# Optimization experiments

Measured on AMD Instinct MI355X. Metric: run time of the kernel, lower is better.

## Reference

```python
import jax, jax.numpy as jnp
import numpy as np

NUM_C = 10000
SEQ_LEN = 1024
EMB = 512
HEADS = 8
NUM_EN = 2
B = 8
HEAD_DIM = EMB // HEADS


def _ln(x, s, b, eps=1e-5):
    m = jnp.mean(x, -1, keepdims=True)
    v = jnp.mean((x - m) ** 2, -1, keepdims=True)
    return (x - m) / jnp.sqrt(v + eps) * s + b


def setup_inputs():
    key = jax.random.key(0)
    k = jax.random.split(key, 16)

    def n(i, shape, scale=0.02):
        return scale * jax.random.normal(k[i], shape, dtype=jnp.float32)

    q = jax.random.randint(k[0], (B, SEQ_LEN), 0, NUM_C)
    r = jax.random.randint(k[1], (B, SEQ_LEN), 0, 2)
    qry = jax.random.randint(k[2], (B, SEQ_LEN), 0, NUM_C)
    alphas = n(3, (SEQ_LEN, 2), 0.001)
    # gumbels = -log(Exp(1) + eps), matching torch's exponential_() sampling
    gumbel = -jnp.log(jax.random.exponential(k[4], (SEQ_LEN, 2), dtype=jnp.float32) + 1e-5)
    # keep offset-0 (the diagonal band) selected so no attention row is fully masked
    gumbel = gumbel.at[0, 0].set(10.0)
    return {
        "q": q, "r": r, "qry": qry,
        "alphas": alphas, "gumbel": gumbel,
        "inter_emb": n(5, (2 * NUM_C, EMB)),
        "ex_emb": n(6, (NUM_C, EMB)),
        "pos_emb": n(7, (SEQ_LEN, EMB)),
        "Wqkv": n(8, (NUM_EN, 3 * EMB, EMB)),
        "bqkv": jnp.zeros((NUM_EN, 3 * EMB), jnp.float32),
        "Wo": n(9, (NUM_EN, EMB, EMB)),
        "bo": jnp.zeros((NUM_EN, EMB), jnp.float32),
        "ln1_s": jnp.ones((NUM_EN, EMB), jnp.float32),
        "ln1_b": jnp.zeros((NUM_EN, EMB), jnp.float32),
        "W1": n(10, (NUM_EN, EMB, EMB)),
        "b1": jnp.zeros((NUM_EN, EMB), jnp.float32),
        "W2": n(11, (NUM_EN, EMB, EMB)),
        "b2": jnp.zeros((NUM_EN, EMB), jnp.float32),
        "ln2_s": jnp.ones((NUM_EN, EMB), jnp.float32),
        "ln2_b": jnp.zeros((NUM_EN, EMB), jnp.float32),
        "pred_w": n(12, (1, EMB)),
        "pred_b": jnp.zeros((1,), jnp.float32),
    }


def reference(q, r, qry, alphas, gumbel, inter_emb, ex_emb, pos_emb, Wqkv, bqkv, Wo, bo,
              ln1_s, ln1_b, W1, b1, W2, b2, ln2_s, ln2_b, pred_w, pred_b):
    L = SEQ_LEN
    x = inter_emb[q + NUM_C * r] + pos_emb[jnp.arange(L)]  # [B,L,E]
    qsh = ex_emb[qry]                                      # [B,L,E]

    # Gumbel-softmax hard top-1 (straight-through); column 0 == "keep" indicator per offset
    y_soft = jax.nn.softmax(alphas + gumbel, axis=-1)      # tau = 1
    y_hard = jax.nn.one_hot(jnp.argmax(y_soft, -1), 2, dtype=y_soft.dtype)
    m = (y_hard - jax.lax.stop_gradient(y_soft) + y_soft)[:, 0]  # [L], 0/1 in fwd

    # The triu/rot90/loop construction collapses to a symmetric Toeplitz: dam[i,j] = m[|i-j|]
    idx = jnp.arange(L)
    dam = m[jnp.abs(idx[:, None] - idx[None, :])]          # [L,L]
    allowed = (idx[None, :] <= idx[:, None]) & (dam != 0)  # causal AND band kept
    bias = jnp.where(allowed, 0.0, -jnp.inf)               # same for all heads

    scale = np.float32(1.0 / np.sqrt(HEAD_DIM))
    for l in range(NUM_EN):
        Wq, Wk, Wv = jnp.split(Wqkv[l], 3, axis=0)
        bq, bk, bv = jnp.split(bqkv[l], 3, axis=0)
        qp = (qsh @ Wq.T + bq).reshape(B, L, HEADS, HEAD_DIM)
        kp = (x @ Wk.T + bk).reshape(B, L, HEADS, HEAD_DIM)
        vp = (x @ Wv.T + bv).reshape(B, L, HEADS, HEAD_DIM)
        scores = jnp.einsum('bihd,bjhd->bhij', qp, kp) * scale + bias
        attn = jax.nn.softmax(scores, axis=-1)
        out = jnp.einsum('bhij,bjhd->bihd', attn, vp).reshape(B, L, EMB)
        out = out @ Wo[l].T + bo[l]
        h = _ln(qsh + out, ln1_s[l], ln1_b[l])             # residual with the query (as in source)
        ff = jax.nn.relu(h @ W1[l].T + b1[l]) @ W2[l].T + b2[l]
        x = _ln(h + ff, ln2_s[l], ln2_b[l])

    p = jax.nn.sigmoid(x @ pred_w.T + pred_b).squeeze(-1)  # [B,L]
    mask_L1 = jnp.sum(jnp.abs(alphas))
    return p, mask_L1
```

## Files before the change

kernel.cpp:

```cpp
#include <hip/hip_runtime.h>
#include <hip/hip_bf16.h>

#define L_SEQ 1024
#define NUMC  10000

typedef __attribute__((ext_vector_type(8))) short bf16x8;
typedef __attribute__((ext_vector_type(4))) float f32x4;

__device__ __forceinline__ unsigned int bf2(float a, float b) {
    unsigned int ua = __float_as_uint(a);
    ua = (ua + 0x7fffu + ((ua >> 16) & 1u)) >> 16;
    unsigned int ub = __float_as_uint(b);
    ub = (ub + 0x7fffu + ((ub >> 16) & 1u)) >> 16;
    return ua | (ub << 16);
}
__device__ __forceinline__ unsigned short bf1(float a) {
    unsigned int ua = __float_as_uint(a);
    return (unsigned short)((ua + 0x7fffu + ((ua >> 16) & 1u)) >> 16);
}

__global__ __launch_bounds__(256) void mask_l1_kernel(
    const float* __restrict__ alphas, const float* __restrict__ gumbel,
    float* __restrict__ msk, float* __restrict__ out)
{
    int tid = threadIdx.x;
    float la = 0.0f;
    #pragma unroll
    for (int rr = 0; rr < 4; ++rr) {
        int i = tid + rr * 256;
        float a0 = alphas[2*i],  a1 = alphas[2*i+1];
        float s0 = a0 + gumbel[2*i], s1 = a1 + gumbel[2*i+1];
        msk[i] = (s0 >= s1) ? 1.0f : 0.0f;
        la += fabsf(a0) + fabsf(a1);
    }
    #pragma unroll
    for (int o = 1; o < 64; o <<= 1) la += __shfl_xor(la, o);
    __shared__ float red[4];
    int lane = tid & 63, wid = tid >> 6;
    if (lane == 0) red[wid] = la;
    __syncthreads();
    if (tid == 0)
        out[8192] = red[0] + red[1] + red[2] + red[3];
}

__global__ __launch_bounds__(128) void embed_x_kernel(
    const int* __restrict__ q, const int* __restrict__ r,
    const float* __restrict__ inter_emb, const float* __restrict__ pos_emb,
    float* __restrict__ x)
{
    int row = blockIdx.x;
    int pos = row & (L_SEQ - 1);
    int t = threadIdx.x;
    int e = q[row] + NUMC * r[row];
    float4 a = ((const float4*)(inter_emb + (size_t)e * 512))[t];
    float4 p = ((const float4*)(pos_emb + (size_t)pos * 512))[t];
    float4 o; o.x=a.x+p.x; o.y=a.y+p.y; o.z=a.z+p.z; o.w=a.w+p.w;
    ((float4*)(x + (size_t)row * 512))[t] = o;
}

__global__ __launch_bounds__(128) void embed_q_kernel(
    const int* __restrict__ qry, const float* __restrict__ ex_emb,
    float* __restrict__ qsh)
{
    int row = blockIdx.x;
    int t = threadIdx.x;
    ((float4*)(qsh + (size_t)row * 512))[t] =
        ((const float4*)(ex_emb + (size_t)qry[row] * 512))[t];
}

__global__ __launch_bounds__(256) void gemm_mfma(
    const float* __restrict__ A, const float* __restrict__ W,
    const float* __restrict__ bias, const float* __restrict__ R,
    void* __restrict__ C_, int c_bf, int ldc, int relu)
{
    __shared__ __align__(16) char lsA[128 * 128];
    __shared__ __align__(16) char lsB[128 * 128];
    int t = threadIdx.x;
    int lane = t & 63, wid = t >> 6;
    int wr = wid >> 1, wc = wid & 1;
    int l15 = lane & 15, l4 = lane >> 4;
    int m0 = blockIdx.y * 128, n0 = blockIdx.x * 128;

    f32x4 zero = {0.f, 0.f, 0.f, 0.f};
    f32x4 acc[4][4];
    #pragma unroll
    for (int i = 0; i < 4; ++i)
        #pragma unroll
        for (int j = 0; j < 4; ++j) acc[i][j] = zero;

    for (int kt = 0; kt < 512; kt += 64) {
        float4 ra[4][2], rb[4][2];
        #pragma unroll
        for (int i = 0; i < 4; ++i) {
            int pp = t + (i << 8);
            int row = pp >> 3, c8 = pp & 7;
            const float* pa = A + (size_t)(m0 + row) * 512 + kt + (c8 << 3);
            ra[i][0] = *(const float4*)pa;
            ra[i][1] = *(const float4*)(pa + 4);
            const float* pb = W + (size_t)(n0 + row) * 512 + kt + (c8 << 3);
            rb[i][0] = *(const float4*)pb;
            rb[i][1] = *(const float4*)(pb + 4);
        }
        __syncthreads();
        #pragma unroll
        for (int i = 0; i < 4; ++i) {
            int pp = t + (i << 8);
            int row = pp >> 3, c8 = pp & 7;
            int byte = ((row << 7) + (c8 << 4)) ^ ((row & 7) << 4);
            uint4 pk;
            pk.x = bf2(ra[i][0].x, ra[i][0].y);
            pk.y = bf2(ra[i][0].z, ra[i][0].w);
            pk.z = bf2(ra[i][1].x, ra[i][1].y);
            pk.w = bf2(ra[i][1].z, ra[i][1].w);
            *(uint4*)(lsA + byte) = pk;
            pk.x = bf2(rb[i][0].x, rb[i][0].y);
            pk.y = bf2(rb[i][0].z, rb[i][0].w);
            pk.z = bf2(rb[i][1].x, rb[i][1].y);
            pk.w = bf2(rb[i][1].z, rb[i][1].w);
            *(uint4*)(lsB + byte) = pk;
        }
        __syncthreads();
        #pragma unroll
        for (int kk = 0; kk < 2; ++kk) {
            bf16x8 af[4], bfv[4];
            #pragma unroll
            for (int i = 0; i < 4; ++i) {
                int rowA = (wr << 6) + (i << 4) + l15;
                int ba = ((rowA << 7) + (kk << 6) + (l4 << 4)) ^ ((rowA & 7) << 4);
                af[i] = *(const bf16x8*)(lsA + ba);
                int rowB = (wc << 6) + (i << 4) + l15;
                int bb = ((rowB << 7) + (kk << 6) + (l4 << 4)) ^ ((rowB & 7) << 4);
                bfv[i] = *(const bf16x8*)(lsB + bb);
            }
            #pragma unroll
            for (int i = 0; i < 4; ++i)
                #pragma unroll
                for (int j = 0; j < 4; ++j)
                    acc[i][j] = __builtin_amdgcn_mfma_f32_16x16x32_bf16(
                        af[i], bfv[j], acc[i][j], 0, 0, 0);
        }
    }
    float bv[4];
    #pragma unroll
    for (int j = 0; j < 4; ++j) bv[j] = bias[n0 + (wc << 6) + (j << 4) + l15];
    #pragma unroll
    for (int i = 0; i < 4; ++i) {
        #pragma unroll
        for (int r = 0; r < 4; ++r) {
            int grow = m0 + (wr << 6) + (i << 4) + (l4 << 2) + r;
            #pragma unroll
            for (int j = 0; j < 4; ++j) {
                int gcol = n0 + (wc << 6) + (j << 4) + l15;
                float o = acc[i][j][r] + bv[j];
                if (R) o += R[(size_t)grow * 512 + gcol];
                if (relu) o = fmaxf(o, 0.0f);
                if (c_bf) ((__hip_bfloat16*)C_)[(size_t)grow * ldc + gcol] = __float2bfloat16(o);
                else      ((float*)C_)[(size_t)grow * ldc + gcol] = o;
            }
        }
    }
}

__global__ __launch_bounds__(256) void attn_mfma(
    const float* __restrict__ qsh, const float* __restrict__ Wq,
    const float* __restrict__ bq, const __hip_bfloat16* __restrict__ KV,
    const float* __restrict__ msk, float* __restrict__ O)
{
    __shared__ __align__(16) char lsK[64 * 128];
    __shared__ __align__(16) char lsV[64 * 128];
    __shared__ __align__(16) char lsQ[64 * 128];
    __shared__ __align__(16) char lsP[64 * 128];
    __shared__ float mskS[L_SEQ];
    int qt = blockIdx.x, h = blockIdx.y, b = blockIdx.z;
    int i0 = qt * 64;
    size_t base = (size_t)b * L_SEQ;
    int t = threadIdx.x;
    int lane = t & 63, w = t >> 6, l15 = lane & 15, l4 = lane >> 4;

    #pragma unroll
    for (int k = 0; k < 4; ++k) mskS[t + k * 256] = msk[t + k * 256];

    f32x4 zero = {0.f, 0.f, 0.f, 0.f};
    f32x4 qa[4];
    #pragma unroll
    for (int j = 0; j < 4; ++j) qa[j] = zero;
    for (int kt = 0; kt < 512; kt += 64) {
        float4 ra[2][2], rb[2][2];
        #pragma unroll
        for (int i = 0; i < 2; ++i) {
            int p = t * 2 + i;
            int row = p >> 3, c8 = p & 7;
            const float* pa = qsh + (base + i0 + row) * 512 + kt + (c8 << 3);
            ra[i][0] = *(const float4*)pa;  ra[i][1] = *(const float4*)(pa + 4);
            const float* pw = Wq + (size_t)(h * 64 + row) * 512 + kt + (c8 << 3);
            rb[i][0] = *(const float4*)pw;  rb[i][1] = *(const float4*)(pw + 4);
        }
        __syncthreads();
        #pragma unroll
        for (int i = 0; i < 2; ++i) {
            int p = t * 2 + i;
            int row = p >> 3, c8 = p & 7;
            int byte = ((row << 7) + (c8 << 4)) ^ ((row & 7) << 4);
            uint4 pk;
            pk.x = bf2(ra[i][0].x, ra[i][0].y); pk.y = bf2(ra[i][0].z, ra[i][0].w);
            pk.z = bf2(ra[i][1].x, ra[i][1].y); pk.w = bf2(ra[i][1].z, ra[i][1].w);
            *(uint4*)(lsK + byte) = pk;
            pk.x = bf2(rb[i][0].x, rb[i][0].y); pk.y = bf2(rb[i][0].z, rb[i][0].w);
            pk.z = bf2(rb[i][1].x, rb[i][1].y); pk.w = bf2(rb[i][1].z, rb[i][1].w);
            *(uint4*)(lsV + byte) = pk;
        }
        __syncthreads();
        #pragma unroll
        for (int kk = 0; kk < 2; ++kk) {
            int ra_ = (w << 4) + l15;
            bf16x8 af = *(const bf16x8*)(lsK + (((ra_ << 7) + (kk << 6) + (l4 << 4)) ^ ((ra_ & 7) << 4)));
            #pragma unroll
            for (int df = 0; df < 4; ++df) {
                int rb_ = (df << 4) + l15;
                bf16x8 bf = *(const bf16x8*)(lsV + (((rb_ << 7) + (kk << 6) + (l4 << 4)) ^ ((rb_ & 7) << 4)));
                qa[df] = __builtin_amdgcn_mfma_f32_16x16x32_bf16(af, bf, qa[df], 0, 0, 0);
            }
        }
    }
    #pragma unroll
    for (int df = 0; df < 4; ++df) {
        float bias = bq[h * 64 + (df << 4) + l15];
        #pragma unroll
        for (int r = 0; r < 4; ++r) {
            int row = (w << 4) + (l4 << 2) + r;
            int byte = ((row << 7) + (((df << 4) + l15) << 1)) ^ ((row & 7) << 4);
            *(unsigned short*)(lsQ + byte) = bf1(qa[df][r] + bias);
        }
    }

    float mcur[4], lcur[4];
    f32x4 oa[4];
    #pragma unroll
    for (int r = 0; r < 4; ++r) { mcur[r] = -INFINITY; lcur[r] = 0.f; }
    #pragma unroll
    for (int df = 0; df < 4; ++df) oa[df] = zero;

    for (int jt = 0; jt <= qt; ++jt) {
        int j0 = jt * 64;
        __syncthreads();
        #pragma unroll
        for (int i = 0; i < 2; ++i) {
            int p = t * 2 + i;
            int row = p >> 3, c8 = p & 7;
            uint4 kv4 = *(const uint4*)(KV + (base + j0 + row) * 1024 + h * 64 + (c8 << 3));
            *(uint4*)(lsK + (((row << 7) + (c8 << 4)) ^ ((row & 7) << 4))) = kv4;
            uint4 vv = *(const uint4*)(KV + (base + j0 + row) * 1024 + 512 + h * 64 + (c8 << 3));
            const unsigned short* vs = (const unsigned short*)&vv;
            #pragma unroll
            for (int e = 0; e < 8; ++e) {
                int d = (c8 << 3) + e;
                *(unsigned short*)(lsV + (((d << 7) + (row << 1)) ^ ((d & 7) << 4))) = vs[e];
            }
        }
        __syncthreads();
        f32x4 s[4];
        #pragma unroll
        for (int jf = 0; jf < 4; ++jf) s[jf] = zero;
        #pragma unroll
        for (int kk = 0; kk < 2; ++kk) {
            int ra_ = (w << 4) + l15;
            bf16x8 af = *(const bf16x8*)(lsQ + (((ra_ << 7) + (kk << 6) + (l4 << 4)) ^ ((ra_ & 7) << 4)));
            #pragma unroll
            for (int jf = 0; jf < 4; ++jf) {
                int rb_ = (jf << 4) + l15;
                bf16x8 bf = *(const bf16x8*)(lsK + (((rb_ << 7) + (kk << 6) + (l4 << 4)) ^ ((rb_ & 7) << 4)));
                s[jf] = __builtin_amdgcn_mfma_f32_16x16x32_bf16(af, bf, s[jf], 0, 0, 0);
            }
        }
        #pragma unroll
        for (int r = 0; r < 4; ++r) {
            int gi = i0 + (w << 4) + (l4 << 2) + r;
            float rm = -INFINITY;
            #pragma unroll
            for (int jf = 0; jf < 4; ++jf) {
                int gj = j0 + (jf << 4) + l15;
                float v = s[jf][r] * 0.125f;
                bool ok = (gj <= gi) && (mskS[gi - gj] != 0.0f);
                v = ok ? v : -INFINITY;
                s[jf][r] = v;
                rm = fmaxf(rm, v);
            }
            #pragma unroll
            for (int o = 1; o < 16; o <<= 1) rm = fmaxf(rm, __shfl_xor(rm, o));
            float mn = fmaxf(mcur[r], rm);
            float c, psum = 0.f;
            if (mn == -INFINITY) {
                c = 1.0f;
                #pragma unroll
                for (int jf = 0; jf < 4; ++jf) s[jf][r] = 0.f;
            } else {
                c = __expf(mcur[r] - mn);
                #pragma unroll
                for (int jf = 0; jf < 4; ++jf) {
                    float e = __expf(s[jf][r] - mn);
                    s[jf][r] = e; psum += e;
                }
            }
            #pragma unroll
            for (int o = 1; o < 16; o <<= 1) psum += __shfl_xor(psum, o);
            mcur[r] = mn;
            lcur[r] = lcur[r] * c + psum;
            #pragma unroll
            for (int df = 0; df < 4; ++df) oa[df][r] *= c;
            int row = (w << 4) + (l4 << 2) + r;
            #pragma unroll
            for (int jf = 0; jf < 4; ++jf) {
                int byte = ((row << 7) + (((jf << 4) + l15) << 1)) ^ ((row & 7) << 4);
                *(unsigned short*)(lsP + byte) = bf1(s[jf][r]);
            }
        }
        __syncthreads();
        #pragma unroll
        for (int kk = 0; kk < 2; ++kk) {
            int ra_ = (w << 4) + l15;
            bf16x8 pf = *(const bf16x8*)(lsP + (((ra_ << 7) + (kk << 6) + (l4 << 4)) ^ ((ra_ & 7) << 4)));
            #pragma unroll
            for (int df = 0; df < 4; ++df) {
                int rb_ = (df << 4) + l15;
                bf16x8 vf = *(const bf16x8*)(lsV + (((rb_ << 7) + (kk << 6) + (l4 << 4)) ^ ((rb_ & 7) << 4)));
                oa[df] = __builtin_amdgcn_mfma_f32_16x16x32_bf16(pf, vf, oa[df], 0, 0, 0);
            }
        }
    }
    #pragma unroll
    for (int r = 0; r < 4; ++r) {
        int gi = i0 + (w << 4) + (l4 << 2) + r;
        float inv = 1.0f / lcur[r];
        #pragma unroll
        for (int df = 0; df < 4; ++df)
            O[(base + gi) * 512 + h * 64 + (df << 4) + l15] = oa[df][r] * inv;
    }
}

__global__ __launch_bounds__(128) void ln_kernel(float* __restrict__ X,
    const float* __restrict__ s, const float* __restrict__ b)
{
    int row = blockIdx.x, t = threadIdx.x;
    float* xp = X + (size_t)row * 512;
    float4 v = *((float4*)xp + t);
    float ps = v.x + v.y + v.z + v.w;
    #pragma unroll
    for (int o = 1; o < 64; o <<= 1) ps += __shfl_xor(ps, o);
    __shared__ float sm[4];
    int lane = t & 63, wid = t >> 6;
    if (lane == 0) sm[wid] = ps;
    __syncthreads();
    float mean = (sm[0] + sm[1]) * (1.0f / 512.0f);
    float4 d; d.x=v.x-mean; d.y=v.y-mean; d.z=v.z-mean; d.w=v.w-mean;
    float sq = d.x*d.x + d.y*d.y + d.z*d.z + d.w*d.w;
    #pragma unroll
    for (int o = 1; o < 64; o <<= 1) sq += __shfl_xor(sq, o);
    if (lane == 0) sm[2 + wid] = sq;
    __syncthreads();
    float inv = rsqrtf((sm[2] + sm[3]) * (1.0f / 512.0f) + 1e-5f);
    float4 sc = *((const float4*)s + t);
    float4 sh = *((const float4*)b + t);
    float4 o;
    o.x = d.x*inv*sc.x + sh.x; o.y = d.y*inv*sc.y + sh.y;
    o.z = d.z*inv*sc.z + sh.z; o.w = d.w*inv*sc.w + sh.w;
    *((float4*)xp + t) = o;
}

__global__ __launch_bounds__(256) void desakt_50629074485961_kernel(
    const float* __restrict__ x, const float* __restrict__ pw,
    const float* __restrict__ pb, float* __restrict__ out)
{
    int row = blockIdx.x * 4 + (threadIdx.x >> 6);
    int lane = threadIdx.x & 63;
    const float4* xr = (const float4*)(x + (size_t)row * 512) + lane * 2;
    const float4* wr = (const float4*)pw + lane * 2;
    float4 a0 = xr[0], a1 = xr[1], w0 = wr[0], w1 = wr[1];
    float s = a0.x*w0.x + a0.y*w0.y + a0.z*w0.z + a0.w*w0.w
            + a1.x*w1.x + a1.y*w1.y + a1.z*w1.z + a1.w*w1.w;
    #pragma unroll
    for (int o = 1; o < 64; o <<= 1) s += __shfl_xor(s, o);
    if (lane == 0) {
        float z = s + pb[0];
        out[row] = 1.0f / (1.0f + __expf(-z));
    }
}

extern "C" __attribute__((visibility("default")))
void kernel_launch(void* const* d_in, const int* in_sizes, int n_in,
                   void* d_out, int out_size, void* d_ws, size_t ws_size,
                   hipStream_t stream) {
    (void)in_sizes; (void)n_in; (void)out_size;
    const int*   q        = (const int*)d_in[0];
    const int*   r        = (const int*)d_in[1];
    const int*   qry      = (const int*)d_in[2];
    const float* alphas   = (const float*)d_in[3];
    const float* gumbel   = (const float*)d_in[4];
    const float* inter_emb= (const float*)d_in[5];
    const float* ex_emb   = (const float*)d_in[6];
    const float* pos_emb  = (const float*)d_in[7];
    const float* Wqkv     = (const float*)d_in[8];
    const float* bqkv     = (const float*)d_in[9];
    const float* Wo       = (const float*)d_in[10];
    const float* bo       = (const float*)d_in[11];
    const float* ln1_s    = (const float*)d_in[12];
    const float* ln1_b    = (const float*)d_in[13];
    const float* W1       = (const float*)d_in[14];
    const float* b1       = (const float*)d_in[15];
    const float* W2       = (const float*)d_in[16];
    const float* b2       = (const float*)d_in[17];
    const float* ln2_s    = (const float*)d_in[18];
    const float* ln2_b    = (const float*)d_in[19];
    const float* pred_w   = (const float*)d_in[20];
    const float* pred_b   = (const float*)d_in[21];
    float* out            = (float*)d_out;

    const size_t NT = 8192;
    const size_t needA = (1024 + 3 * NT * 512) * 4 + NT * 1024 * 2;
    float *msk, *x, *qsh, *t;
    __hip_bfloat16* kv;
    if (ws_size >= needA) {
        msk = (float*)d_ws;
        x   = msk + 1024;
        qsh = x   + NT * 512;
        t   = qsh + NT * 512;
        kv  = (__hip_bfloat16*)(t + NT * 512);
    } else {
        msk = (float*)d_ws;
        x   = msk + 1024;
        qsh = (float*)inter_emb;
        t   = qsh + NT * 512;
        kv  = (__hip_bfloat16*)ex_emb;
    }

    mask_l1_kernel<<<1, 256, 0, stream>>>(alphas, gumbel, msk, out);
    embed_x_kernel<<<8192, 128, 0, stream>>>(q, r, inter_emb, pos_emb, x);
    embed_q_kernel<<<8192, 128, 0, stream>>>(qry, ex_emb, qsh);

    for (int l = 0; l < 2; ++l) {
        const float* Wl = Wqkv + (size_t)l * 1536 * 512;
        const float* bl = bqkv + (size_t)l * 1536;
        gemm_mfma<<<dim3(8, 64), 256, 0, stream>>>(x, Wl + 512 * 512, bl + 512,
                                                   nullptr, kv, 1, 1024, 0);
        attn_mfma<<<dim3(16, 8, 8), 256, 0, stream>>>(qsh, Wl, bl, kv, msk, t);
        gemm_mfma<<<dim3(4, 64), 256, 0, stream>>>(t, Wo + (size_t)l * 512 * 512,
                                                   bo + l * 512, qsh, x, 0, 512, 0);
        ln_kernel<<<8192, 128, 0, stream>>>(x, ln1_s + l * 512, ln1_b + l * 512);
        gemm_mfma<<<dim3(4, 64), 256, 0, stream>>>(x, W1 + (size_t)l * 512 * 512,
                                                   b1 + l * 512, nullptr, t, 0, 512, 1);
        gemm_mfma<<<dim3(4, 64), 256, 0, stream>>>(t, W2 + (size_t)l * 512 * 512,
                                                   b2 + l * 512, x, x, 0, 512, 0);
        ln_kernel<<<8192, 128, 0, stream>>>(x, ln2_s + l * 512, ln2_b + l * 512);
    }
    desakt_50629074485961_kernel<<<2048, 256, 0, stream>>>(x, pred_w, pred_b, out);
}
```

Baseline: 710.0 us.

## Pair causal query tiles per block and precompute Q projection in separate GEMM

The Q projection is moved out of the attention kernel into a standalone bf16 GEMM. Before, every (query tile, head, batch) block recomputed its head's Q from fp32 inputs. The attention kernel now processes two query tiles per block (tile qp and 15-qp), so each block does the same causal work and shares each K/V tile load between both. This halves the grid, doubles shared memory and accumulator registers per block, and adds an extra kernel launch plus a bf16 Q buffer in workspace.

```diff
diff --git a/kernel.cpp b/kernel.cpp
--- a/kernel.cpp
+++ b/kernel.cpp
@@ -161,92 +161,116 @@
     }
 }
 
+__device__ __forceinline__ void online_sm(
+    f32x4 s[4], int i0, int j0, int w, int l4, int l15,
+    const float* mskS, float mcur[4], float lcur[4], f32x4 oa[4], char* lsP)
+{
+    #pragma unroll
+    for (int r = 0; r < 4; ++r) {
+        int gi = i0 + (w << 4) + (l4 << 2) + r;
+        float rm = -INFINITY;
+        #pragma unroll
+        for (int jf = 0; jf < 4; ++jf) {
+            int gj = j0 + (jf << 4) + l15;
+            float v = s[jf][r] * 0.125f;
+            bool ok = (gj <= gi) && (mskS[gi - gj] != 0.0f);
+            v = ok ? v : -INFINITY;
+            s[jf][r] = v;
+            rm = fmaxf(rm, v);
+        }
+        #pragma unroll
+        for (int o = 1; o < 16; o <<= 1) rm = fmaxf(rm, __shfl_xor(rm, o));
+        float mn = fmaxf(mcur[r], rm);
+        float c, psum = 0.f;
+        if (mn == -INFINITY) {
+            c = 1.0f;
+            #pragma unroll
+            for (int jf = 0; jf < 4; ++jf) s[jf][r] = 0.f;
+        } else {
+            c = __expf(mcur[r] - mn);
+            #pragma unroll
+            for (int jf = 0; jf < 4; ++jf) {
+                float e = __expf(s[jf][r] - mn);
+                s[jf][r] = e; psum += e;
+            }
+        }
+        #pragma unroll
+        for (int o = 1; o < 16; o <<= 1) psum += __shfl_xor(psum, o);
+        mcur[r] = mn;
+        lcur[r] = lcur[r] * c + psum;
+        #pragma unroll
+        for (int df = 0; df < 4; ++df) oa[df][r] *= c;
+        int row = (w << 4) + (l4 << 2) + r;
+        #pragma unroll
+        for (int jf = 0; jf < 4; ++jf) {
+            int byte = ((row << 7) + (((jf << 4) + l15) << 1)) ^ ((row & 7) << 4);
+            *(unsigned short*)(lsP + byte) = bf1(s[jf][r]);
+        }
+    }
+}
+
+__device__ __forceinline__ void pv_acc(
+    const char* lsP, const char* lsV, int w, int l4, int l15, f32x4 oa[4])
+{
+    #pragma unroll
+    for (int kk = 0; kk < 2; ++kk) {
+        int ra_ = (w << 4) + l15;
+        bf16x8 pf = *(const bf16x8*)(lsP + (((ra_ << 7) + (kk << 6) + (l4 << 4)) ^ ((ra_ & 7) << 4)));
+        #pragma unroll
+        for (int df = 0; df < 4; ++df) {
+            int rb_ = (df << 4) + l15;
+            bf16x8 vf = *(const bf16x8*)(lsV + (((rb_ << 7) + (kk << 6) + (l4 << 4)) ^ ((rb_ & 7) << 4)));
+            oa[df] = __builtin_amdgcn_mfma_f32_16x16x32_bf16(pf, vf, oa[df], 0, 0, 0);
+        }
+    }
+}
+
 __global__ __launch_bounds__(256) void attn_mfma(
-    const float* __restrict__ qsh, const float* __restrict__ Wq,
-    const float* __restrict__ bq, const __hip_bfloat16* __restrict__ KV,
+    const __hip_bfloat16* __restrict__ Qg, const __hip_bfloat16* __restrict__ KV,
     const float* __restrict__ msk, float* __restrict__ O)
 {
+    __shared__ __align__(16) char lsQA[64 * 128];
+    __shared__ __align__(16) char lsQB[64 * 128];
     __shared__ __align__(16) char lsK[64 * 128];
     __shared__ __align__(16) char lsV[64 * 128];
-    __shared__ __align__(16) char lsQ[64 * 128];
-    __shared__ __align__(16) char lsP[64 * 128];
+    __shared__ __align__(16) char lsPA[64 * 128];
+    __shared__ __align__(16) char lsPB[64 * 128];
     __shared__ float mskS[L_SEQ];
-    int qt = blockIdx.x, h = blockIdx.y, b = blockIdx.z;
-    int i0 = qt * 64;
+    int qp = blockIdx.x, h = blockIdx.y, b = blockIdx.z;
+    int qtA = qp, qtB = 15 - qp;
+    int i0A = qtA * 64, i0B = qtB * 64;
     size_t base = (size_t)b * L_SEQ;
     int t = threadIdx.x;
     int lane = t & 63, w = t >> 6, l15 = lane & 15, l4 = lane >> 4;
 
     #pragma unroll
     for (int k = 0; k < 4; ++k) mskS[t + k * 256] = msk[t + k * 256];
+    #pragma unroll
+    for (int i = 0; i < 2; ++i) {
+        int idx = t * 2 + i;
+        int row = idx >> 3, c16 = idx & 7;
+        int byte = ((row << 7) + (c16 << 4)) ^ ((row & 7) << 4);
+        *(uint4*)(lsQA + byte) =
+            *(const uint4*)(Qg + (base + i0A + row) * 512 + h * 64 + (c16 << 3));
+        *(uint4*)(lsQB + byte) =
+            *(const uint4*)(Qg + (base + i0B + row) * 512 + h * 64 + (c16 << 3));
+    }
 
     f32x4 zero = {0.f, 0.f, 0.f, 0.f};
-    f32x4 qa[4];
-    #pragma unroll
-    for (int j = 0; j < 4; ++j) qa[j] = zero;
-    for (int kt = 0; kt < 512; kt += 64) {
-        float4 ra[2][2], rb[2][2];
-        #pragma unroll
-        for (int i = 0; i < 2; ++i) {
-            int p = t * 2 + i;
-            int row = p >> 3, c8 = p & 7;
-            const float* pa = qsh + (base + i0 + row) * 512 + kt + (c8 << 3);
-            ra[i][0] = *(const float4*)pa;  ra[i][1] = *(const float4*)(pa + 4);
-            const float* pw = Wq + (size_t)(h * 64 + row) * 512 + kt + (c8 << 3);
-            rb[i][0] = *(const float4*)pw;  rb[i][1] = *(const float4*)(pw + 4);
-        }
-        __syncthreads();
-        #pragma unroll
-        for (int i = 0; i < 2; ++i) {
-            int p = t * 2 + i;
-            int row = p >> 3, c8 = p & 7;
-            int byte = ((row << 7) + (c8 << 4)) ^ ((row & 7) << 4);
-            uint4 pk;
-            pk.x = bf2(ra[i][0].x, ra[i][0].y); pk.y = bf2(ra[i][0].z, ra[i][0].w);
-            pk.z = bf2(ra[i][1].x, ra[i][1].y); pk.w = bf2(ra[i][1].z, ra[i][1].w);
-            *(uint4*)(lsK + byte) = pk;
-            pk.x = bf2(rb[i][0].x, rb[i][0].y); pk.y = bf2(rb[i][0].z, rb[i][0].w);
-            pk.z = bf2(rb[i][1].x, rb[i][1].y); pk.w = bf2(rb[i][1].z, rb[i][1].w);
-            *(uint4*)(lsV + byte) = pk;
-        }
-        __syncthreads();
-        #pragma unroll
-        for (int kk = 0; kk < 2; ++kk) {
-            int ra_ = (w << 4) + l15;
-            bf16x8 af = *(const bf16x8*)(lsK + (((ra_ << 7) + (kk << 6) + (l4 << 4)) ^ ((ra_ & 7) << 4)));
-            #pragma unroll
-            for (int df = 0; df < 4; ++df) {
-                int rb_ = (df << 4) + l15;
-                bf16x8 bf = *(const bf16x8*)(lsV + (((rb_ << 7) + (kk << 6) + (l4 << 4)) ^ ((rb_ & 7) << 4)));
-                qa[df] = __builtin_amdgcn_mfma_f32_16x16x32_bf16(af, bf, qa[df], 0, 0, 0);
-            }
-        }
-    }
-    #pragma unroll
-    for (int df = 0; df < 4; ++df) {
-        float bias = bq[h * 64 + (df << 4) + l15];
-        #pragma unroll
-        for (int r = 0; r < 4; ++r) {
-            int row = (w << 4) + (l4 << 2) + r;
-            int byte = ((row << 7) + (((df << 4) + l15) << 1)) ^ ((row & 7) << 4);
-            *(unsigned short*)(lsQ + byte) = bf1(qa[df][r] + bias);
-        }
-    }
-
-    float mcur[4], lcur[4];
-    f32x4 oa[4];
-    #pragma unroll
-    for (int r = 0; r < 4; ++r) { mcur[r] = -INFINITY; lcur[r] = 0.f; }
-    #pragma unroll
-    for (int df = 0; df < 4; ++df) oa[df] = zero;
-
-    for (int jt = 0; jt <= qt; ++jt) {
+    float mA[4], lA[4], mB[4], lB[4];
+    f32x4 oaA[4], oaB[4];
+    #pragma unroll
+    for (int r = 0; r < 4; ++r) { mA[r] = mB[r] = -INFINITY; lA[r] = lB[r] = 0.f; }
+    #pragma unroll
+    for (int df = 0; df < 4; ++df) { oaA[df] = zero; oaB[df] = zero; }
+
+    for (int jt = 0; jt <= qtB; ++jt) {
         int j0 = jt * 64;
         __syncthreads();
         #pragma unroll
         for (int i = 0; i < 2; ++i) {
-            int p = t * 2 + i;
-            int row = p >> 3, c8 = p & 7;
+            int idx = t * 2 + i;
+            int row = idx >> 3, c8 = idx & 7;
             uint4 kv4 = *(const uint4*)(KV + (base + j0 + row) * 1024 + h * 64 + (c8 << 3));
             *(uint4*)(lsK + (((row << 7) + (c8 << 4)) ^ ((row & 7) << 4))) = kv4;
             uint4 vv = *(const uint4*)(KV + (base + j0 + row) * 1024 + 512 + h * 64 + (c8 << 3));
@@ -258,82 +282,54 @@
             }
         }
         __syncthreads();
-        f32x4 s[4];
-        #pragma unroll
-        for (int jf = 0; jf < 4; ++jf) s[jf] = zero;
-        #pragma unroll
-        for (int kk = 0; kk < 2; ++kk) {
-            int ra_ = (w << 4) + l15;
-            bf16x8 af = *(const bf16x8*)(lsQ + (((ra_ << 7) + (kk << 6) + (l4 << 4)) ^ ((ra_ & 7) << 4)));
-            #pragma unroll
-            for (int jf = 0; jf < 4; ++jf) {
-                int rb_ = (jf << 4) + l15;
-                bf16x8 bf = *(const bf16x8*)(lsK + (((rb_ << 7) + (kk << 6) + (l4 << 4)) ^ ((rb_ & 7) << 4)));
-                s[jf] = __builtin_amdgcn_mfma_f32_16x16x32_bf16(af, bf, s[jf], 0, 0, 0);
-            }
-        }
-        #pragma unroll
-        for (int r = 0; r < 4; ++r) {
-            int gi = i0 + (w << 4) + (l4 << 2) + r;
-            float rm = -INFINITY;
-            #pragma unroll
-            for (int jf = 0; jf < 4; ++jf) {
-                int gj = j0 + (jf << 4) + l15;
-                float v = s[jf][r] * 0.125f;
-                bool ok = (gj <= gi) && (mskS[gi - gj] != 0.0f);
-                v = ok ? v : -INFINITY;
-                s[jf][r] = v;
-                rm = fmaxf(rm, v);
-            }
-            #pragma unroll
-            for (int o = 1; o < 16; o <<= 1) rm = fmaxf(rm, __shfl_xor(rm, o));
-            float mn = fmaxf(mcur[r], rm);
-            float c, psum = 0.f;
-            if (mn == -INFINITY) {
-                c = 1.0f;
-                #pragma unroll
-                for (int jf = 0; jf < 4; ++jf) s[jf][r] = 0.f;
-            } else {
-                c = __expf(mcur[r] - mn);
+        {
+            f32x4 s[4];
+            #pragma unroll
+            for (int jf = 0; jf < 4; ++jf) s[jf] = zero;
+            #pragma unroll
+            for (int kk = 0; kk < 2; ++kk) {
+                int ra_ = (w << 4) + l15;
+                bf16x8 af = *(const bf16x8*)(lsQB + (((ra_ << 7) + (kk << 6) + (l4 << 4)) ^ ((ra_ & 7) << 4)));
                 #pragma unroll
                 for (int jf = 0; jf < 4; ++jf) {
-                    float e = __expf(s[jf][r] - mn);
-                    s[jf][r] = e; psum += e;
+                    int rb_ = (jf << 4) + l15;
+                    bf16x8 bf = *(const bf16x8*)(lsK + (((rb_ << 7) + (kk << 6) + (l4 << 4)) ^ ((rb_ & 7) << 4)));
+                    s[jf] = __builtin_amdgcn_mfma_f32_16x16x32_bf16(af, bf, s[jf], 0, 0, 0);
                 }
             }
-            #pragma unroll
-            for (int o = 1; o < 16; o <<= 1) psum += __shfl_xor(psum, o);
-            mcur[r] = mn;
-            lcur[r] = lcur[r] * c + psum;
-            #pragma unroll
-            for (int df = 0; df < 4; ++df) oa[df][r] *= c;
-            int row = (w << 4) + (l4 << 2) + r;
-            #pragma unroll
-            for (int jf = 0; jf < 4; ++jf) {
-                int byte = ((row << 7) + (((jf << 4) + l15) << 1)) ^ ((row & 7) << 4);
-                *(unsigned short*)(lsP + byte) = bf1(s[jf][r]);
-            }
+            online_sm(s, i0B, j0, w, l4, l15, mskS, mB, lB, oaB, lsPB);
+        }
+        if (jt <= qtA) {
+            f32x4 s[4];
+            #pragma unroll
+            for (int jf = 0; jf < 4; ++jf) s[jf] = zero;
+            #pragma unroll
+            for (int kk = 0; kk < 2; ++kk) {
+                int ra_ = (w << 4) + l15;
+                bf16x8 af = *(const bf16x8*)(lsQA + (((ra_ << 7) + (kk << 6) + (l4 << 4)) ^ ((ra_ & 7) << 4)));
+                #pragma unroll
+                for (int jf = 0; jf < 4; ++jf) {
+                    int rb_ = (jf << 4) + l15;
+                    bf16x8 bf = *(const bf16x8*)(lsK + (((rb_ << 7) + (kk << 6) + (l4 << 4)) ^ ((rb_ & 7) << 4)));
+                    s[jf] = __builtin_amdgcn_mfma_f32_16x16x32_bf16(af, bf, s[jf], 0, 0, 0);
+                }
+            }
+            online_sm(s, i0A, j0, w, l4, l15, mskS, mA, lA, oaA, lsPA);
         }
         __syncthreads();
-        #pragma unroll
-        for (int kk = 0; kk < 2; ++kk) {
-            int ra_ = (w << 4) + l15;
-            bf16x8 pf = *(const bf16x8*)(lsP + (((ra_ << 7) + (kk << 6) + (l4 << 4)) ^ ((ra_ & 7) << 4)));
-            #pragma unroll
-            for (int df = 0; df < 4; ++df) {
-                int rb_ = (df << 4) + l15;
-                bf16x8 vf = *(const bf16x8*)(lsV + (((rb_ << 7) + (kk << 6) + (l4 << 4)) ^ ((rb_ & 7) << 4)));
-                oa[df] = __builtin_amdgcn_mfma_f32_16x16x32_bf16(pf, vf, oa[df], 0, 0, 0);
-            }
-        }
+        pv_acc(lsPB, lsV, w, l4, l15, oaB);
+        if (jt <= qtA) pv_acc(lsPA, lsV, w, l4, l15, oaA);
     }
     #pragma unroll
     for (int r = 0; r < 4; ++r) {
-        int gi = i0 + (w << 4) + (l4 << 2) + r;
-        float inv = 1.0f / lcur[r];
-        #pragma unroll
-        for (int df = 0; df < 4; ++df)
-            O[(base + gi) * 512 + h * 64 + (df << 4) + l15] = oa[df][r] * inv;
+        int giA = i0A + (w << 4) + (l4 << 2) + r;
+        int giB = i0B + (w << 4) + (l4 << 2) + r;
+        float invA = 1.0f / lA[r], invB = 1.0f / lB[r];
+        #pragma unroll
+        for (int df = 0; df < 4; ++df) {
+            O[(base + giA) * 512 + h * 64 + (df << 4) + l15] = oaA[df][r] * invA;
+            O[(base + giB) * 512 + h * 64 + (df << 4) + l15] = oaB[df][r] * invB;
+        }
     }
 }
 
@@ -415,21 +411,23 @@
     float* out            = (float*)d_out;
 
     const size_t NT = 8192;
-    const size_t needA = (1024 + 3 * NT * 512) * 4 + NT * 1024 * 2;
+    const size_t needA = (1024 + 3 * NT * 512) * 4 + NT * 512 * 2 + NT * 1024 * 2;
     float *msk, *x, *qsh, *t;
-    __hip_bfloat16* kv;
+    __hip_bfloat16 *qb, *kvb;
     if (ws_size >= needA) {
         msk = (float*)d_ws;
         x   = msk + 1024;
         qsh = x   + NT * 512;
         t   = qsh + NT * 512;
-        kv  = (__hip_bfloat16*)(t + NT * 512);
+        qb  = (__hip_bfloat16*)(t + NT * 512);
+        kvb = qb + NT * 512;
     } else {
         msk = (float*)d_ws;
         x   = msk + 1024;
         qsh = (float*)inter_emb;
         t   = qsh + NT * 512;
-        kv  = (__hip_bfloat16*)ex_emb;
+        qb  = (__hip_bfloat16*)(t + NT * 512);
+        kvb = (__hip_bfloat16*)ex_emb;
     }
 
     mask_l1_kernel<<<1, 256, 0, stream>>>(alphas, gumbel, msk, out);
@@ -439,9 +437,10 @@
     for (int l = 0; l < 2; ++l) {
         const float* Wl = Wqkv + (size_t)l * 1536 * 512;
         const float* bl = bqkv + (size_t)l * 1536;
+        gemm_mfma<<<dim3(4, 64), 256, 0, stream>>>(qsh, Wl, bl, nullptr, qb, 1, 512, 0);
         gemm_mfma<<<dim3(8, 64), 256, 0, stream>>>(x, Wl + 512 * 512, bl + 512,
-                                                   nullptr, kv, 1, 1024, 0);
-        attn_mfma<<<dim3(16, 8, 8), 256, 0, stream>>>(qsh, Wl, bl, kv, msk, t);
+                                                   nullptr, kvb, 1, 1024, 0);
+        attn_mfma<<<dim3(8, 8, 8), 256, 0, stream>>>(qb, kvb, msk, t);
         gemm_mfma<<<dim3(4, 64), 256, 0, stream>>>(t, Wo + (size_t)l * 512 * 512,
                                                    bo + l * 512, qsh, x, 0, 512, 0);
         ln_kernel<<<8192, 128, 0, stream>>>(x, ln1_s + l * 512, ln1_b + l * 512);
```

New measurement: 632.0 us. -11.0%, faster.
